# Kernel optimization log

Hardware: AMD Instinct MI355X
Metric: run time of the kernel (lower is better)

The kernel has to match this reference:

```python
import jax, jax.numpy as jnp
import numpy as np

N_NODES = 100000   # n_all_trajs
N_EDGES = 640000
HIDDEN = 128
N_USERS = 1000


def gcn_conv(x, edge_index, edge_weight, W, b, num_nodes):
    """PyG GCNConv with add_self_loops=False, normalize=True.
    out[col] += (deg^-1/2[row] * w * deg^-1/2[col]) * (x @ W)[row]; then + b.
    deg is weighted in-degree at the target (col) nodes."""
    row, col = edge_index[0], edge_index[1]
    deg = jax.ops.segment_sum(edge_weight, col, num_segments=num_nodes)
    deg_inv_sqrt = jnp.where(deg > 0, jax.lax.rsqrt(jnp.maximum(deg, 1e-30)), 0.0)
    norm = deg_inv_sqrt[row] * edge_weight * deg_inv_sqrt[col]   # [E]
    h = x @ W                                                    # [N, H]
    msg = h[row] * norm[:, None]                                 # [E, H] gather+scale
    out = jax.ops.segment_sum(msg, col, num_segments=num_nodes)  # scatter-add
    return out + b


def setup_inputs() -> dict:
    key = jax.random.key(0)
    ks = jax.random.split(key, 9)
    edge_index = jax.random.randint(ks[0], (2, N_EDGES), 0, N_NODES, dtype=jnp.int64)
    edge_weight = jax.random.uniform(ks[1], (N_EDGES,), dtype=jnp.float32)
    emb = jax.random.normal(ks[2], (N_NODES, HIDDEN), dtype=jnp.float32) * 0.02
    W1 = jax.random.normal(ks[3], (HIDDEN, HIDDEN), dtype=jnp.float32) * 0.05
    b1 = jax.random.normal(ks[4], (HIDDEN,), dtype=jnp.float32) * 0.01
    W2 = jax.random.normal(ks[5], (HIDDEN, HIDDEN), dtype=jnp.float32) * 0.05
    b2 = jax.random.normal(ks[6], (HIDDEN,), dtype=jnp.float32) * 0.01
    Wp = jax.random.normal(ks[7], (HIDDEN, N_USERS), dtype=jnp.float32) * 0.05
    bp = jax.random.normal(ks[8], (N_USERS,), dtype=jnp.float32) * 0.01
    return {"edge_index": edge_index, "edge_weight": edge_weight, "emb": emb,
            "W1": W1, "b1": b1, "W2": W2, "b2": b2, "Wp": Wp, "bp": bp}


def reference(edge_index, edge_weight, emb, W1, b1, W2, b2, Wp, bp):
    h1 = gcn_conv(emb, edge_index, edge_weight, W1, b1, N_NODES)
    # dropout p=0.0 (inference) -> identity
    h2 = gcn_conv(h1, edge_index, edge_weight, W2, b2, N_NODES)
    predictions = h2 @ Wp + bp   # [N_NODES, N_USERS]
    return predictions
```

## Files before the change

kernel.cpp:

```cpp
#include <hip/hip_runtime.h>

#define N_NODES 100000
#define N_EDGES 640000
#define HIDDEN  128
#define N_USERS 1000
#define CAP     64

using u16 = unsigned short;
using u32 = unsigned int;

using short8  = __attribute__((ext_vector_type(8))) short;
using floatx4 = __attribute__((ext_vector_type(4))) float;

__device__ __forceinline__ u16 f2bf(float f) {
  u32 u = __float_as_uint(f);
  u32 r = u + 0x7FFFu + ((u >> 16) & 1u);
  return (u16)(r >> 16);
}
__device__ __forceinline__ u32 pack2bf(float a, float b) {
  return (u32)f2bf(a) | ((u32)f2bf(b) << 16);
}
__device__ __forceinline__ float bflo2f(u32 v) { return __uint_as_float(v << 16); }

__global__ void conv_wT(const float* __restrict__ W, u16* __restrict__ BT, int N, int total) {
  int idx = blockIdx.x * 256 + threadIdx.x;
  if (idx >= total) return;
  int n = idx >> 7, k = idx & 127;
  float v = (n < N) ? W[(size_t)k * N + n] : 0.f;
  BT[idx] = f2bf(v);
}

__global__ void deg_kernel(const int* __restrict__ col, const float* __restrict__ w,
                           float* __restrict__ deg, int E) {
  int i = blockIdx.x * 256 + threadIdx.x;
  if (i < E) atomicAdd(&deg[col[i]], w[i]);
}

__global__ void dis_kernel(const float* __restrict__ deg, float* __restrict__ dis, int M) {
  int i = blockIdx.x * 256 + threadIdx.x;
  if (i < M) {
    float d = deg[i];
    dis[i] = d > 0.f ? rsqrtf(d) : 0.f;
  }
}

__global__ void bucket_kernel(const int* __restrict__ row, const int* __restrict__ col,
                              const float* __restrict__ w, const float* __restrict__ dis,
                              int* __restrict__ counts, int2* __restrict__ pairs, int E) {
  int i = blockIdx.x * 256 + threadIdx.x;
  if (i >= E) return;
  int r = row[i], c = col[i];
  int pos = atomicAdd(&counts[c], 1);
  if (pos < CAP) {
    pairs[((size_t)c << 6) + (size_t)pos] = make_int2(r, __float_as_int(dis[r] * w[i] * dis[c]));
  }
}

__global__ __launch_bounds__(256)
void agg_kernel(const u16* __restrict__ hb, const int* __restrict__ counts,
                const int2* __restrict__ pairs,
                const float* __restrict__ bias, u16* __restrict__ out, int M) {
  int wid  = threadIdx.x >> 6;
  int lane = threadIdx.x & 63;
  int n = blockIdx.x * 4 + wid;
  if (n >= M) return;
  int cnt = counts[n];
  cnt = cnt < CAP ? cnt : CAP;
  int2 my = pairs[((size_t)n << 6) + lane];
  int   sv = my.x;
  float wv = __int_as_float(my.y);
  const u32* h32 = (const u32*)hb;
  float ax = 0.f, ay = 0.f;
  int e = 0;
  for (; e + 4 <= cnt; e += 4) {
    int   s0 = __shfl(sv, e),     s1 = __shfl(sv, e + 1);
    int   s2 = __shfl(sv, e + 2), s3 = __shfl(sv, e + 3);
    float w0 = __shfl(wv, e),     w1 = __shfl(wv, e + 1);
    float w2 = __shfl(wv, e + 2), w3 = __shfl(wv, e + 3);
    u32 h0 = h32[((size_t)s0 << 6) + lane];
    u32 h1 = h32[((size_t)s1 << 6) + lane];
    u32 h2 = h32[((size_t)s2 << 6) + lane];
    u32 h3 = h32[((size_t)s3 << 6) + lane];
    ax += w0 * bflo2f(h0 & 0xFFFFu); ay += w0 * __uint_as_float(h0 & 0xFFFF0000u);
    ax += w1 * bflo2f(h1 & 0xFFFFu); ay += w1 * __uint_as_float(h1 & 0xFFFF0000u);
    ax += w2 * bflo2f(h2 & 0xFFFFu); ay += w2 * __uint_as_float(h2 & 0xFFFF0000u);
    ax += w3 * bflo2f(h3 & 0xFFFFu); ay += w3 * __uint_as_float(h3 & 0xFFFF0000u);
  }
  for (; e < cnt; ++e) {
    int   s = __shfl(sv, e);
    float w = __shfl(wv, e);
    u32 hv = h32[((size_t)s << 6) + lane];
    ax += w * bflo2f(hv & 0xFFFFu);
    ay += w * __uint_as_float(hv & 0xFFFF0000u);
  }
  float2 b = ((const float2*)bias)[lane];
  u32 lo = (u32)f2bf(ax + b.x);
  u32 hi = (u32)f2bf(ay + b.y);
  ((u32*)out)[((size_t)n << 6) + lane] = lo | (hi << 16);
}

template<bool F32OUT, bool AF32>
__global__ __launch_bounds__(256, 2)
void gemm_mfma(const void* __restrict__ Av, const u16* __restrict__ BT,
               float* __restrict__ outf, u16* __restrict__ outb,
               const float* __restrict__ bias,
               int M, int Nstore, int ldout) {
  __shared__ u16 As[128 * 128];
  __shared__ u16 Bs[128 * 128];
  const int m0 = blockIdx.x * 128;
  const int n0 = blockIdx.y * 128;
  const int tid = threadIdx.x;

  for (int i = 0; i < 8; ++i) {
    int chunk = tid + i * 256;
    int row = chunk >> 4;
    int c   = chunk & 15;
    int sw  = ((c ^ (row & 15)) << 3);
    int gr  = m0 + row;
    uint4 av = {0u, 0u, 0u, 0u};
    if (gr < M) {
      if (AF32) {
        const float4* s4 = (const float4*)((const float*)Av + ((size_t)gr << 7) + (c << 3));
        float4 lo = s4[0], hi = s4[1];
        av.x = pack2bf(lo.x, lo.y); av.y = pack2bf(lo.z, lo.w);
        av.z = pack2bf(hi.x, hi.y); av.w = pack2bf(hi.z, hi.w);
      } else {
        av = *(const uint4*)((const u16*)Av + ((size_t)gr << 7) + (c << 3));
      }
    }
    *(uint4*)(&As[(row << 7) + sw]) = av;
    uint4 bv = *(const uint4*)(BT + ((size_t)(n0 + row) << 7) + (c << 3));
    *(uint4*)(&Bs[(row << 7) + sw]) = bv;
  }
  __syncthreads();

  const int wid  = tid >> 6, lane = tid & 63;
  const int wr = (wid >> 1) << 6;
  const int wc = (wid & 1) << 6;
  const int lm = lane & 15, quad = lane >> 4;

  floatx4 acc[4][4] = {};
  for (int ks = 0; ks < 4; ++ks) {
    int cks = ks * 4 + quad;
    int sw  = ((cks ^ lm) << 3);
    short8 a[4], b[4];
    for (int i = 0; i < 4; ++i)
      a[i] = *(const short8*)(&As[((wr + i * 16 + lm) << 7) + sw]);
    for (int j = 0; j < 4; ++j)
      b[j] = *(const short8*)(&Bs[((wc + j * 16 + lm) << 7) + sw]);
    for (int i = 0; i < 4; ++i)
      for (int j = 0; j < 4; ++j)
        acc[i][j] = __builtin_amdgcn_mfma_f32_16x16x32_bf16(a[i], b[j], acc[i][j], 0, 0, 0);
  }

  for (int i = 0; i < 4; ++i) {
    int rb = m0 + wr + i * 16 + quad * 4;
    for (int j = 0; j < 4; ++j) {
      int col = n0 + wc + j * 16 + lm;
      if (col < Nstore) {
        float bv = F32OUT ? bias[col] : 0.f;
        for (int r = 0; r < 4; ++r) {
          int row = rb + r;
          if (row < M) {
            float v = acc[i][j][r];
            if (F32OUT) outf[(size_t)row * ldout + col] = v + bv;
            else        outb[((size_t)row << 7) + col]  = f2bf(v);
          }
        }
      }
    }
  }
}

extern "C" void kernel_launch(void* const* d_in, const int* in_sizes, int n_in,
                              void* d_out, int out_size, void* d_ws, size_t ws_size,
                              hipStream_t stream) {
  const int*   eidx = (const int*)d_in[0];
  const int*   erow = eidx;
  const int*   ecol = eidx + N_EDGES;
  const float* ew   = (const float*)d_in[1];
  const float* emb  = (const float*)d_in[2];
  const float* W1   = (const float*)d_in[3];
  const float* b1   = (const float*)d_in[4];
  const float* W2   = (const float*)d_in[5];
  const float* b2   = (const float*)d_in[6];
  const float* Wp   = (const float*)d_in[7];
  const float* bp   = (const float*)d_in[8];
  float* out = (float*)d_out;

  const int M = N_NODES, E = N_EDGES;

  char* p = (char*)d_ws;
  float* deg    = (float*)p;  p += 400128;
  int*   counts = (int*)p;    p += 400128;
  float* dis    = (float*)p;  p += 400128;
  int2*  pairs  = (int2*)p;   p += (size_t)M * CAP * 8;
  u16*   g1     = (u16*)p;    p += (size_t)M * 128 * 2;
  u16*   g2     = (u16*)p;    p += (size_t)M * 128 * 2;
  u16*   W1b    = (u16*)p;    p += 128 * 128 * 2;
  u16*   W2b    = (u16*)p;    p += 128 * 128 * 2;
  u16*   WpT    = (u16*)p;    p += 1024 * 128 * 2;

  hipMemsetAsync(deg, 0, 400128 + 400128, stream);

  conv_wT<<<64,  256, 0, stream>>>(W1, W1b, 128, 128 * 128);
  conv_wT<<<64,  256, 0, stream>>>(W2, W2b, 128, 128 * 128);
  conv_wT<<<512, 256, 0, stream>>>(Wp, WpT, N_USERS, 1024 * 128);

  deg_kernel<<<(E + 255) / 256, 256, 0, stream>>>(ecol, ew, deg, E);
  dis_kernel<<<(M + 255) / 256, 256, 0, stream>>>(deg, dis, M);
  bucket_kernel<<<(E + 255) / 256, 256, 0, stream>>>(erow, ecol, ew, dis, counts, pairs, E);

  const int mt = (M + 127) / 128;
  gemm_mfma<false, true><<<dim3(mt, 1), 256, 0, stream>>>(emb, W1b, nullptr, g1, nullptr, M, 128, 128);
  agg_kernel<<<(M + 3) / 4, 256, 0, stream>>>(g1, counts, pairs, b1, g2, M);
  gemm_mfma<false, false><<<dim3(mt, 1), 256, 0, stream>>>(g2, W2b, nullptr, g1, nullptr, M, 128, 128);
  agg_kernel<<<(M + 3) / 4, 256, 0, stream>>>(g1, counts, pairs, b2, g2, M);
  gemm_mfma<true, false><<<dim3(mt, 8), 256, 0, stream>>>(g2, WpT, out, nullptr, bp, M, N_USERS, N_USERS);
}
```

Baseline: 800.2 us.

## Fold all linear layers into one combined weight applied after aggregation

Because GCN aggregation is linear, the change aggregates raw embeddings twice and then applies a single precomputed weight W1·W2·Wp in the final GEMM. Bias terms are folded in as a per-row scalar (the sum of normalized edge weights) times a vector plus a constant vector. This removes the two 128x128 GEMM passes over 100k nodes. The cost is small weight-combining kernels, a separate cast pass, and different bf16 rounding points. The final GEMM grid is also flattened to 1D with column tiles adjacent.

```diff
diff --git a/kernel.cpp b/kernel.cpp
--- a/kernel.cpp
+++ b/kernel.cpp
@@ -22,12 +22,56 @@
 }
 __device__ __forceinline__ float bflo2f(u32 v) { return __uint_as_float(v << 16); }
 
-__global__ void conv_wT(const float* __restrict__ W, u16* __restrict__ BT, int N, int total) {
+
+__global__ void wcomb1(const float* __restrict__ W1, const float* __restrict__ b1,
+                       const float* __restrict__ W2,
+                       float* __restrict__ T1, float* __restrict__ t1) {
   int idx = blockIdx.x * 256 + threadIdx.x;
-  if (idx >= total) return;
-  int n = idx >> 7, k = idx & 127;
-  float v = (n < N) ? W[(size_t)k * N + n] : 0.f;
-  BT[idx] = f2bf(v);
+  if (idx >= 129 * 128) return;
+  int k = idx >> 7, c = idx & 127;
+  const float* src = (k < 128) ? (W1 + (size_t)k * 128) : b1;
+  float s = 0.f;
+  for (int j = 0; j < 128; ++j) s += src[j] * W2[(size_t)j * 128 + c];
+  if (k < 128) T1[(size_t)k * 128 + c] = s;
+  else         t1[c] = s;
+}
+
+__global__ void wcomb2(const float* __restrict__ T1, const float* __restrict__ Wp,
+                       u16* __restrict__ WcT) {
+  int idx = blockIdx.x * 256 + threadIdx.x;
+  int c = idx >> 7, k = idx & 127;
+  float s = 0.f;
+  if (c < N_USERS)
+    for (int l = 0; l < 128; ++l) s += T1[(size_t)k * 128 + l] * Wp[(size_t)l * N_USERS + c];
+  WcT[idx] = f2bf(s);
+}
+
+__global__ void wcomb3(const float* __restrict__ t1, const float* __restrict__ b2,
+                       const float* __restrict__ Wp, const float* __restrict__ bp,
+                       float* __restrict__ u, float* __restrict__ v) {
+  int idx = blockIdx.x * 256 + threadIdx.x;
+  if (idx >= 2 * N_USERS) return;
+  if (idx < N_USERS) {
+    float s = 0.f;
+    for (int j = 0; j < 128; ++j) s += t1[j] * Wp[(size_t)j * N_USERS + idx];
+    u[idx] = s;
+  } else {
+    int c = idx - N_USERS;
+    float s = bp[c];
+    for (int j = 0; j < 128; ++j) s += b2[j] * Wp[(size_t)j * N_USERS + c];
+    v[c] = s;
+  }
+}
+
+__global__ void cast_kernel(const float* __restrict__ x, u16* __restrict__ xb, int total8) {
+  int i = blockIdx.x * 256 + threadIdx.x;
+  if (i >= total8) return;
+  const float4* s4 = (const float4*)(x + (size_t)i * 8);
+  float4 lo = s4[0], hi = s4[1];
+  uint4 o;
+  o.x = pack2bf(lo.x, lo.y); o.y = pack2bf(lo.z, lo.w);
+  o.z = pack2bf(hi.x, hi.y); o.w = pack2bf(hi.z, hi.w);
+  ((uint4*)xb)[i] = o;
 }
 
 __global__ void deg_kernel(const int* __restrict__ col, const float* __restrict__ w,
@@ -56,29 +100,31 @@
   }
 }
 
+template<bool S1OUT>
 __global__ __launch_bounds__(256)
 void agg_kernel(const u16* __restrict__ hb, const int* __restrict__ counts,
-                const int2* __restrict__ pairs,
-                const float* __restrict__ bias, u16* __restrict__ out, int M) {
+                const int2* __restrict__ pairs, float* __restrict__ s1,
+                u16* __restrict__ out, int M) {
   int wid  = threadIdx.x >> 6;
   int lane = threadIdx.x & 63;
   int n = blockIdx.x * 4 + wid;
   if (n >= M) return;
   int cnt = counts[n];
   cnt = cnt < CAP ? cnt : CAP;
-  int2 my = pairs[((size_t)n << 6) + lane];
+  int2 my = make_int2(0, 0);
+  if (lane < cnt) my = pairs[((size_t)n << 6) + lane];
   int   sv = my.x;
   float wv = __int_as_float(my.y);
   const u32* h32 = (const u32*)hb;
   float ax = 0.f, ay = 0.f;
   int e = 0;
   for (; e + 4 <= cnt; e += 4) {
-    int   s0 = __shfl(sv, e),     s1 = __shfl(sv, e + 1);
-    int   s2 = __shfl(sv, e + 2), s3 = __shfl(sv, e + 3);
-    float w0 = __shfl(wv, e),     w1 = __shfl(wv, e + 1);
-    float w2 = __shfl(wv, e + 2), w3 = __shfl(wv, e + 3);
+    int   s0 = __shfl(sv, e),     s1_ = __shfl(sv, e + 1);
+    int   s2 = __shfl(sv, e + 2), s3  = __shfl(sv, e + 3);
+    float w0 = __shfl(wv, e),     w1  = __shfl(wv, e + 1);
+    float w2 = __shfl(wv, e + 2), w3  = __shfl(wv, e + 3);
     u32 h0 = h32[((size_t)s0 << 6) + lane];
-    u32 h1 = h32[((size_t)s1 << 6) + lane];
+    u32 h1 = h32[((size_t)s1_ << 6) + lane];
     u32 h2 = h32[((size_t)s2 << 6) + lane];
     u32 h3 = h32[((size_t)s3 << 6) + lane];
     ax += w0 * bflo2f(h0 & 0xFFFFu); ay += w0 * __uint_as_float(h0 & 0xFFFF0000u);
@@ -93,22 +139,24 @@
     ax += w * bflo2f(hv & 0xFFFFu);
     ay += w * __uint_as_float(hv & 0xFFFF0000u);
   }
-  float2 b = ((const float2*)bias)[lane];
-  u32 lo = (u32)f2bf(ax + b.x);
-  u32 hi = (u32)f2bf(ay + b.y);
+  if (S1OUT) {
+    float t = wv;
+    for (int o = 32; o; o >>= 1) t += __shfl_xor(t, o);
+    if (lane == 0) s1[n] = t;
+  }
+  u32 lo = (u32)f2bf(ax);
+  u32 hi = (u32)f2bf(ay);
   ((u32*)out)[((size_t)n << 6) + lane] = lo | (hi << 16);
 }
 
-template<bool F32OUT, bool AF32>
 __global__ __launch_bounds__(256, 2)
-void gemm_mfma(const void* __restrict__ Av, const u16* __restrict__ BT,
-               float* __restrict__ outf, u16* __restrict__ outb,
-               const float* __restrict__ bias,
-               int M, int Nstore, int ldout) {
+void gemm_final(const u16* __restrict__ A, const u16* __restrict__ BT,
+                const float* __restrict__ s1, const float* __restrict__ u,
+                const float* __restrict__ vv, float* __restrict__ outf, int M) {
   __shared__ u16 As[128 * 128];
   __shared__ u16 Bs[128 * 128];
-  const int m0 = blockIdx.x * 128;
-  const int n0 = blockIdx.y * 128;
+  const int m0 = (blockIdx.x >> 3) * 128;
+  const int n0 = (blockIdx.x & 7) * 128;
   const int tid = threadIdx.x;
 
   for (int i = 0; i < 8; ++i) {
@@ -118,16 +166,7 @@
     int sw  = ((c ^ (row & 15)) << 3);
     int gr  = m0 + row;
     uint4 av = {0u, 0u, 0u, 0u};
-    if (gr < M) {
-      if (AF32) {
-        const float4* s4 = (const float4*)((const float*)Av + ((size_t)gr << 7) + (c << 3));
-        float4 lo = s4[0], hi = s4[1];
-        av.x = pack2bf(lo.x, lo.y); av.y = pack2bf(lo.z, lo.w);
-        av.z = pack2bf(hi.x, hi.y); av.w = pack2bf(hi.z, hi.w);
-      } else {
-        av = *(const uint4*)((const u16*)Av + ((size_t)gr << 7) + (c << 3));
-      }
-    }
+    if (gr < M) av = *(const uint4*)(A + ((size_t)gr << 7) + (c << 3));
     *(uint4*)(&As[(row << 7) + sw]) = av;
     uint4 bv = *(const uint4*)(BT + ((size_t)(n0 + row) << 7) + (c << 3));
     *(uint4*)(&Bs[(row << 7) + sw]) = bv;
@@ -155,17 +194,16 @@
 
   for (int i = 0; i < 4; ++i) {
     int rb = m0 + wr + i * 16 + quad * 4;
+    float sr[4];
+    for (int r = 0; r < 4; ++r) sr[r] = (rb + r < M) ? s1[rb + r] : 0.f;
     for (int j = 0; j < 4; ++j) {
       int col = n0 + wc + j * 16 + lm;
-      if (col < Nstore) {
-        float bv = F32OUT ? bias[col] : 0.f;
+      if (col < N_USERS) {
+        float uc = u[col], vc = vv[col];
         for (int r = 0; r < 4; ++r) {
           int row = rb + r;
-          if (row < M) {
-            float v = acc[i][j][r];
-            if (F32OUT) outf[(size_t)row * ldout + col] = v + bv;
-            else        outb[((size_t)row << 7) + col]  = f2bf(v);
-          }
+          if (row < M)
+            outf[(size_t)row * N_USERS + col] = acc[i][j][r] + sr[r] * uc + vc;
         }
       }
     }
@@ -195,26 +233,30 @@
   int*   counts = (int*)p;    p += 400128;
   float* dis    = (float*)p;  p += 400128;
   int2*  pairs  = (int2*)p;   p += (size_t)M * CAP * 8;
-  u16*   g1     = (u16*)p;    p += (size_t)M * 128 * 2;
-  u16*   g2     = (u16*)p;    p += (size_t)M * 128 * 2;
-  u16*   W1b    = (u16*)p;    p += 128 * 128 * 2;
-  u16*   W2b    = (u16*)p;    p += 128 * 128 * 2;
-  u16*   WpT    = (u16*)p;    p += 1024 * 128 * 2;
+  u16*   Xb     = (u16*)p;    p += (size_t)M * 128 * 2;
+  u16*   g      = (u16*)p;    p += (size_t)M * 128 * 2;
+  float* T1     = (float*)p;  p += 128 * 128 * 4;
+  float* t1     = (float*)p;  p += 512;
+  u16*   WcT    = (u16*)p;    p += 1024 * 128 * 2;
+  float* uvec   = (float*)p;  p += 4096;
+  float* vvec   = (float*)p;  p += 4096;
+  float* s1     = dis;
 
   hipMemsetAsync(deg, 0, 400128 + 400128, stream);
 
-  conv_wT<<<64,  256, 0, stream>>>(W1, W1b, 128, 128 * 128);
-  conv_wT<<<64,  256, 0, stream>>>(W2, W2b, 128, 128 * 128);
-  conv_wT<<<512, 256, 0, stream>>>(Wp, WpT, N_USERS, 1024 * 128);
+  wcomb1<<<65,  256, 0, stream>>>(W1, b1, W2, T1, t1);
+  wcomb2<<<512, 256, 0, stream>>>(T1, Wp, WcT);
+  wcomb3<<<8,   256, 0, stream>>>(t1, b2, Wp, bp, uvec, vvec);
+
+  cast_kernel<<<(M * 16 + 255) / 256, 256, 0, stream>>>(emb, Xb, M * 16);
 
   deg_kernel<<<(E + 255) / 256, 256, 0, stream>>>(ecol, ew, deg, E);
   dis_kernel<<<(M + 255) / 256, 256, 0, stream>>>(deg, dis, M);
   bucket_kernel<<<(E + 255) / 256, 256, 0, stream>>>(erow, ecol, ew, dis, counts, pairs, E);
 
+  agg_kernel<true ><<<(M + 3) / 4, 256, 0, stream>>>(Xb, counts, pairs, s1, g, M);
+  agg_kernel<false><<<(M + 3) / 4, 256, 0, stream>>>(g,  counts, pairs, nullptr, Xb, M);
+
   const int mt = (M + 127) / 128;
-  gemm_mfma<false, true><<<dim3(mt, 1), 256, 0, stream>>>(emb, W1b, nullptr, g1, nullptr, M, 128, 128);
-  agg_kernel<<<(M + 3) / 4, 256, 0, stream>>>(g1, counts, pairs, b1, g2, M);
-  gemm_mfma<false, false><<<dim3(mt, 1), 256, 0, stream>>>(g2, W2b, nullptr, g1, nullptr, M, 128, 128);
-  agg_kernel<<<(M + 3) / 4, 256, 0, stream>>>(g1, counts, pairs, b2, g2, M);
-  gemm_mfma<true, false><<<dim3(mt, 8), 256, 0, stream>>>(g2, WpT, out, nullptr, bp, M, N_USERS, N_USERS);
-}
+  gemm_final<<<mt * 8, 256, 0, stream>>>(Xb, WcT, s1, uvec, vvec, out, M);
+}
```

New measurement: 790.5 us. Within noise of the previous version (-1.2%).
